# Optimization experiments

Hardware: AMD Instinct MI355X
Metric: run time of the kernel (lower is better)

The kernel has to match this reference:

```python
import jax, jax.numpy as jnp
import numpy as np

EPS = 1e-8  # torch F.cosine_similarity default eps


def setup_inputs() -> dict:
    key = jax.random.key(0)
    ks = jax.random.split(key, 8)
    B, N, D, H = 2, 256, 256, 8
    LEN = 2 * D + 4  # flag == 1
    query = jax.random.normal(ks[0], (B, N, N, D), dtype=jnp.float32)
    k_in = jax.random.normal(ks[1], (B, N, N, D), dtype=jnp.float32)
    s_query = jax.random.uniform(ks[2], (B, N, N, 2), dtype=jnp.float32)
    s_key = jax.random.uniform(ks[3], (B, N, N, 2), dtype=jnp.float32)
    roi_mask = jnp.ones((B, N, N), dtype=jnp.float32)
    # nn.Linear(LEN, H) params
    bound = 1.0 / np.sqrt(LEN)
    W = jax.random.uniform(ks[4], (H, LEN), minval=-bound, maxval=bound, dtype=jnp.float32)
    b_lin = jax.random.uniform(ks[5], (H,), minval=-bound, maxval=bound, dtype=jnp.float32)
    return {"query": query, "key": k_in, "s_query": s_query, "s_key": s_key,
            "roi_mask": roi_mask, "W": W, "b_lin": b_lin, "node_num": 32}


def reference(query, key, s_query, s_key, roi_mask, W, b_lin, node_num):
    B, N, _, D = query.shape
    # spatial feature for flag==1: simple concat
    spat = jnp.concatenate([s_query, s_key], axis=3)          # (B,N,N,4)
    ft = jnp.concatenate([query, key, spat], axis=3)          # (B,N,N,2D+4)
    attn1 = jax.nn.sigmoid(jnp.einsum('bqkc,hc->bqkh', ft, W) + b_lin)  # (B,N,N,H)

    # cosine-similarity scores over channel dim, then relu (Attention_4)
    qn = jnp.maximum(jnp.sqrt(jnp.sum(query * query, axis=3)), EPS)
    kn = jnp.maximum(jnp.sqrt(jnp.sum(key * key, axis=3)), EPS)
    scores = jnp.sum(query * key, axis=3) / (qn * kn)         # (B,N,N)
    attn = jax.nn.relu(scores)

    # torch: values, idces = topk(attn(B,N,N,1), node_num, dim=2);
    #        atten_mask[:, :, idces, :] = 1.0
    # Fancy indexing with the full idces tensor sets dim-2 position p to 1
    # for ALL (b, row) whenever p appears ANYWHERE in idces -> a global
    # indicator vector along dim 2.
    _, idces = jax.lax.top_k(attn, node_num)                  # (B,N,node_num)
    ind = jnp.zeros((N,), dtype=attn1.dtype).at[idces.reshape(-1)].set(1.0)

    out = attn1 * roi_mask[:, :, :, None] * ind[None, None, :, None]
    return out
```

## Files before the change

kernel.cpp:

```cpp
#include <hip/hip_runtime.h>

#define NPAIR 131072
#define NDIM  256
#define NH    8
#define NN    256
#define NROWS 512
#define LEN   516
#define EPSV  1e-8f

__device__ __forceinline__ float dot4(float4 a, float4 b) {
    return fmaf(a.x, b.x, fmaf(a.y, b.y, fmaf(a.z, b.z, a.w * b.w)));
}

#define DPP_ADD(x, ctrl)                                                        \
    x += __int_as_float(__builtin_amdgcn_update_dpp(                            \
        0, __float_as_int(x), (ctrl), 0xf, 0xf, false))

__device__ __forceinline__ float wave_sum63(float x) {
    DPP_ADD(x, 0x111);
    DPP_ADD(x, 0x112);
    DPP_ADD(x, 0x114);
    DPP_ADD(x, 0x118);
    DPP_ADD(x, 0x142);
    DPP_ADD(x, 0x143);
    return x;
}

__global__ __launch_bounds__(256, 4) void fused_main(
    const float* __restrict__ Q, const float* __restrict__ K,
    const float* __restrict__ SQ, const float* __restrict__ SK,
    const float* __restrict__ ROI, const float* __restrict__ W,
    const float* __restrict__ Bb, float* __restrict__ out,
    float* __restrict__ scores)
{
    const int lane = threadIdx.x & 63;
    const int h = lane & 7;
    const int nwaves = (gridDim.x * blockDim.x) >> 6;
    const int wave = (blockIdx.x * blockDim.x + threadIdx.x) >> 6;

    const float4* __restrict__ Q4 = (const float4*)Q;
    const float4* __restrict__ K4 = (const float4*)K;

    float4 wq[NH], wk[NH];
#pragma unroll
    for (int i = 0; i < NH; i++) {
        wq[i] = *(const float4*)(W + i * LEN + lane * 4);
        wk[i] = *(const float4*)(W + i * LEN + 256 + lane * 4);
    }
    const float4 wt = *(const float4*)(W + h * LEN + 512);
    const float bh = Bb[h];

    for (int p0 = wave; p0 < NPAIR; p0 += nwaves) {
        const int p = __builtin_amdgcn_readfirstlane(p0);
        const float4 qv = Q4[(size_t)p * 64 + lane];
        const float4 kv = K4[(size_t)p * 64 + lane];

        float r[11];
        r[8]  = dot4(qv, kv);
        r[9]  = dot4(qv, qv);
        r[10] = dot4(kv, kv);
#pragma unroll
        for (int i = 0; i < NH; i++)
            r[i] = dot4(qv, wq[i]) + dot4(kv, wk[i]);

#pragma unroll
        for (int i = 0; i < 11; i++)
            r[i] = wave_sum63(r[i]);

        if (lane == 63) {
            const float qn = fmaxf(sqrtf(r[9]),  EPSV);
            const float kn = fmaxf(sqrtf(r[10]), EPSV);
            scores[p] = fmaxf(r[8] / (qn * kn), 0.0f);
        }

        float hs = 0.0f;
#pragma unroll
        for (int i = 0; i < NH; i++) {
            const float si = __int_as_float(
                __builtin_amdgcn_readlane(__float_as_int(r[i]), 63));
            hs = (h == i) ? si : hs;
        }

        const float2 sq = ((const float2*)SQ)[p];
        const float2 sk = ((const float2*)SK)[p];
        const float roi = ROI[p];
        const float x = hs + sq.x * wt.x + sq.y * wt.y
                           + sk.x * wt.z + sk.y * wt.w + bh;
        const float y = roi / (1.0f + __expf(-x));
        if (lane < NH) out[(size_t)p * NH + lane] = y;
    }
}

__global__ void zero_ind(float* __restrict__ ind) {
    ind[threadIdx.x] = 0.0f;
}

__global__ __launch_bounds__(64) void topk_kernel(
    const float* __restrict__ scores, float* __restrict__ ind,
    const int* __restrict__ node_num)
{
    const int row = blockIdx.x;
    const int lane = threadIdx.x;
    const float4 v4 = *(const float4*)(scores + row * NN + lane * 4);
    float v[4] = {v4.x, v4.y, v4.z, v4.w};

    int Kk = node_num[0];
    if (Kk > NN) Kk = NN;
    for (int t = 0; t < Kk; t++) {
        float mv = v[0];
        int mi = lane * 4;
#pragma unroll
        for (int j = 1; j < 4; j++) {
            if (v[j] > mv) { mv = v[j]; mi = lane * 4 + j; }
        }
        for (int off = 32; off > 0; off >>= 1) {
            const float ov = __shfl_xor(mv, off, 64);
            const int   oi = __shfl_xor(mi, off, 64);
            if (ov > mv || (ov == mv && oi < mi)) { mv = ov; mi = oi; }
        }
        if (lane == 0) ind[mi] = 1.0f;
        if ((mi >> 2) == lane) v[mi & 3] = -1.0f;
    }
}

__global__ __launch_bounds__(256) void apply_ind_kernel(
    float* __restrict__ out, const float* __restrict__ ind)
{
    const int i = blockIdx.x * blockDim.x + threadIdx.x;
    float4 v = ((float4*)out)[i];
    const float m = ind[(i >> 1) & (NN - 1)];
    v.x *= m; v.y *= m; v.z *= m; v.w *= m;
    ((float4*)out)[i] = v;
}

extern "C" void kernel_launch(void* const* d_in, const int* in_sizes, int n_in,
                              void* d_out, int out_size, void* d_ws, size_t ws_size,
                              hipStream_t stream)
{
    const float* Q   = (const float*)d_in[0];
    const float* K   = (const float*)d_in[1];
    const float* SQ  = (const float*)d_in[2];
    const float* SK  = (const float*)d_in[3];
    const float* ROI = (const float*)d_in[4];
    const float* W   = (const float*)d_in[5];
    const float* Bb  = (const float*)d_in[6];
    const int* node_num = (const int*)d_in[7];

    float* out = (float*)d_out;
    float* scores = (float*)d_ws;
    float* ind = scores + NPAIR;

    fused_main<<<2048, 256, 0, stream>>>(Q, K, SQ, SK, ROI, W, Bb, out, scores);
    zero_ind<<<1, 256, 0, stream>>>(ind);
    topk_kernel<<<NROWS, 64, 0, stream>>>(scores, ind, node_num);
    apply_ind_kernel<<<out_size / 4 / 256, 256, 0, stream>>>(out, ind);
}
```

Before: 322.0 us.

## Compute dot products and linear projection with bf16 MFMA over 16-pair tiles

Replaces the per-pair wave reduction (one pair per wave, DPP reductions of 11 partial sums) with MFMA 16x16x32 bf16 instructions processing 16 pairs per wave. The q·k, q·q and k·k products are read from the diagonal of the MFMA outputs, and the 8-head projection is accumulated via MFMA against bf16-packed weights. This removes the cross-lane reduction overhead, but it rounds inputs to bf16, which changes numerics for both the cosine scores that feed top-k and the attention outputs. The grid is halved and the launch bound hint is dropped.

```diff
diff --git a/kernel.cpp b/kernel.cpp
--- a/kernel.cpp
+++ b/kernel.cpp
@@ -1,93 +1,104 @@
 #include <hip/hip_runtime.h>
+#include <hip/hip_bf16.h>
 
 #define NPAIR 131072
-#define NDIM  256
+#define NUNIT 8192
 #define NH    8
 #define NN    256
 #define NROWS 512
 #define LEN   516
 #define EPSV  1e-8f
 
-__device__ __forceinline__ float dot4(float4 a, float4 b) {
-    return fmaf(a.x, b.x, fmaf(a.y, b.y, fmaf(a.z, b.z, a.w * b.w)));
+typedef __attribute__((ext_vector_type(8))) short bf16x8;
+typedef __attribute__((ext_vector_type(4))) float f32x4;
+
+__device__ __forceinline__ unsigned int pk2(float x, float y) {
+    union { __hip_bfloat162 h; unsigned int u; } c;
+    c.h = __float22bfloat162_rn(make_float2(x, y));
+    return c.u;
+}
+__device__ __forceinline__ bf16x8 pack8(float4 a, float4 b) {
+    union { unsigned int u[4]; bf16x8 v; } r;
+    r.u[0] = pk2(a.x, a.y);
+    r.u[1] = pk2(a.z, a.w);
+    r.u[2] = pk2(b.x, b.y);
+    r.u[3] = pk2(b.z, b.w);
+    return r.v;
 }
 
-#define DPP_ADD(x, ctrl)                                                        \
-    x += __int_as_float(__builtin_amdgcn_update_dpp(                            \
-        0, __float_as_int(x), (ctrl), 0xf, 0xf, false))
-
-__device__ __forceinline__ float wave_sum63(float x) {
-    DPP_ADD(x, 0x111);
-    DPP_ADD(x, 0x112);
-    DPP_ADD(x, 0x114);
-    DPP_ADD(x, 0x118);
-    DPP_ADD(x, 0x142);
-    DPP_ADD(x, 0x143);
-    return x;
-}
-
-__global__ __launch_bounds__(256, 4) void fused_main(
+__global__ void fused_main(
     const float* __restrict__ Q, const float* __restrict__ K,
     const float* __restrict__ SQ, const float* __restrict__ SK,
     const float* __restrict__ ROI, const float* __restrict__ W,
     const float* __restrict__ Bb, float* __restrict__ out,
     float* __restrict__ scores)
 {
-    const int lane = threadIdx.x & 63;
-    const int h = lane & 7;
+    const int l    = threadIdx.x & 63;
+    const int quad = l >> 4;
+    const int m    = l & 15;
+    const int hh   = m & 7;
+    const int koff = quad * 8;
     const int nwaves = (gridDim.x * blockDim.x) >> 6;
     const int wave = (blockIdx.x * blockDim.x + threadIdx.x) >> 6;
 
-    const float4* __restrict__ Q4 = (const float4*)Q;
-    const float4* __restrict__ K4 = (const float4*)K;
+    bf16x8 wqf[8], wkf[8];
+#pragma unroll
+    for (int c = 0; c < 8; ++c) {
+        const float* wp = W + hh * LEN + c * 32 + koff;
+        wqf[c] = pack8(*(const float4*)wp,        *(const float4*)(wp + 4));
+        wkf[c] = pack8(*(const float4*)(wp + 256), *(const float4*)(wp + 260));
+    }
+    const float4 wt = *(const float4*)(W + hh * LEN + 512);
+    const float bh = Bb[hh];
 
-    float4 wq[NH], wk[NH];
-#pragma unroll
-    for (int i = 0; i < NH; i++) {
-        wq[i] = *(const float4*)(W + i * LEN + lane * 4);
-        wk[i] = *(const float4*)(W + i * LEN + 256 + lane * 4);
-    }
-    const float4 wt = *(const float4*)(W + h * LEN + 512);
-    const float bh = Bb[h];
+    const bool diag_owner = ((m >> 2) == quad);
+    const int  dreg = m & 3;
 
-    for (int p0 = wave; p0 < NPAIR; p0 += nwaves) {
-        const int p = __builtin_amdgcn_readfirstlane(p0);
-        const float4 qv = Q4[(size_t)p * 64 + lane];
-        const float4 kv = K4[(size_t)p * 64 + lane];
+    for (int u = wave; u < NUNIT; u += nwaves) {
+        const int p0 = u * 16;
+        const float* qbase = Q + (size_t)(p0 + m) * 256 + koff;
+        const float* kbase = K + (size_t)(p0 + m) * 256 + koff;
 
-        float r[11];
-        r[8]  = dot4(qv, kv);
-        r[9]  = dot4(qv, qv);
-        r[10] = dot4(kv, kv);
-#pragma unroll
-        for (int i = 0; i < NH; i++)
-            r[i] = dot4(qv, wq[i]) + dot4(kv, wk[i]);
+        f32x4 a_qk = {0.f, 0.f, 0.f, 0.f};
+        f32x4 a_qq = {0.f, 0.f, 0.f, 0.f};
+        f32x4 a_kk = {0.f, 0.f, 0.f, 0.f};
+        f32x4 a_pr = {0.f, 0.f, 0.f, 0.f};
 
 #pragma unroll
-        for (int i = 0; i < 11; i++)
-            r[i] = wave_sum63(r[i]);
-
-        if (lane == 63) {
-            const float qn = fmaxf(sqrtf(r[9]),  EPSV);
-            const float kn = fmaxf(sqrtf(r[10]), EPSV);
-            scores[p] = fmaxf(r[8] / (qn * kn), 0.0f);
+        for (int c = 0; c < 8; ++c) {
+            const float4 qa = *(const float4*)(qbase + c * 32);
+            const float4 qb = *(const float4*)(qbase + c * 32 + 4);
+            const float4 ka = *(const float4*)(kbase + c * 32);
+            const float4 kb = *(const float4*)(kbase + c * 32 + 4);
+            const bf16x8 qf = pack8(qa, qb);
+            const bf16x8 kf = pack8(ka, kb);
+            a_qk = __builtin_amdgcn_mfma_f32_16x16x32_bf16(qf, kf, a_qk, 0, 0, 0);
+            a_qq = __builtin_amdgcn_mfma_f32_16x16x32_bf16(qf, qf, a_qq, 0, 0, 0);
+            a_kk = __builtin_amdgcn_mfma_f32_16x16x32_bf16(kf, kf, a_kk, 0, 0, 0);
+            a_pr = __builtin_amdgcn_mfma_f32_16x16x32_bf16(qf, wqf[c], a_pr, 0, 0, 0);
+            a_pr = __builtin_amdgcn_mfma_f32_16x16x32_bf16(kf, wkf[c], a_pr, 0, 0, 0);
         }
 
-        float hs = 0.0f;
-#pragma unroll
-        for (int i = 0; i < NH; i++) {
-            const float si = __int_as_float(
-                __builtin_amdgcn_readlane(__float_as_int(r[i]), 63));
-            hs = (h == i) ? si : hs;
+        if (diag_owner) {
+            const float qk = a_qk[dreg];
+            const float qq = a_qq[dreg];
+            const float kk = a_kk[dreg];
+            const float d = fmaxf(sqrtf(qq), EPSV) * fmaxf(sqrtf(kk), EPSV);
+            scores[p0 + m] = fmaxf(qk / d, 0.0f);
         }
 
-        const float2 sq = ((const float2*)SQ)[p];
-        const float2 sk = ((const float2*)SK)[p];
-        const float roi = ROI[p];
-        const float x = hs + sq.x * wt.x + sq.y * wt.y
-                           + sk.x * wt.z + sk.y * wt.w + bh;
-        const float y = roi / (1.0f + __expf(-x));
-        if (lane < NH) out[(size_t)p * NH + lane] = y;
+        if (m < NH) {
+#pragma unroll
+            for (int r = 0; r < 4; ++r) {
+                const int p = p0 + quad * 4 + r;
+                const float2 sq = ((const float2*)SQ)[p];
+                const float2 sk = ((const float2*)SK)[p];
+                const float roi = ROI[p];
+                const float x = a_pr[r] + sq.x * wt.x + sq.y * wt.y
+                                        + sk.x * wt.z + sk.y * wt.w + bh;
+                out[(size_t)p * NH + m] = roi / (1.0f + __expf(-x));
+            }
+        }
     }
 }
 
@@ -150,7 +161,7 @@
     float* scores = (float*)d_ws;
     float* ind = scores + NPAIR;
 
-    fused_main<<<2048, 256, 0, stream>>>(Q, K, SQ, SK, ROI, W, Bb, out, scores);
+    fused_main<<<1024, 256, 0, stream>>>(Q, K, SQ, SK, ROI, W, Bb, out, scores);
     zero_ind<<<1, 256, 0, stream>>>(ind);
     topk_kernel<<<NROWS, 64, 0, stream>>>(scores, ind, node_num);
     apply_ind_kernel<<<out_size / 4 / 256, 256, 0, stream>>>(out, ind);
```

New measurement: 320.0 us. No clear change (-0.6%).
